# Performance work log

Measured on AMD Instinct MI355X. Metric: run time of the kernel, lower is better.

## Reference

```python
import jax, jax.numpy as jnp
import numpy as np

DEPTH, HEADS, DIM, DHEAD, MLP = 4, 16, 1024, 64, 4096
B, N, M = 4, 1024, 1024
EPS = 1e-5


def layer_norm(x, w, b):
    mu = jnp.mean(x, axis=-1, keepdims=True)
    var = jnp.var(x, axis=-1, keepdims=True)
    return (x - mu) * jax.lax.rsqrt(var + EPS) * w + b


def setup_inputs() -> dict:
    key = jax.random.key(0)
    ks = jax.random.split(key, 16)
    inner = HEADS * DHEAD
    s = lambda fan_in: 1.0 / np.sqrt(fan_in)
    # weights stored in (in, out) layout: y = x @ W + b
    return {
        "x": jax.random.normal(ks[0], (B, N, DIM), jnp.float32),
        "m": jax.random.normal(ks[1], (B, M, DIM), jnp.float32),
        "Wq": jax.random.normal(ks[2], (DEPTH, DIM, inner), jnp.float32) * s(DIM),
        "Wk": jax.random.normal(ks[3], (DEPTH, DIM, inner), jnp.float32) * s(DIM),
        "Wv": jax.random.normal(ks[4], (DEPTH, DIM, inner), jnp.float32) * s(DIM),
        "Wo": jax.random.normal(ks[5], (DEPTH, inner, DIM), jnp.float32) * s(inner),
        "bo": jnp.zeros((DEPTH, DIM), jnp.float32),
        "ln1_w": jnp.ones((DEPTH, DIM), jnp.float32),
        "ln1_b": jnp.zeros((DEPTH, DIM), jnp.float32),
        "W1": jax.random.normal(ks[6], (DEPTH, DIM, MLP), jnp.float32) * s(DIM),
        "b1": jnp.zeros((DEPTH, MLP), jnp.float32),
        "W2": jax.random.normal(ks[7], (DEPTH, MLP, DIM), jnp.float32) * s(MLP),
        "b2": jnp.zeros((DEPTH, DIM), jnp.float32),
        "ln2_w": jnp.ones((DEPTH, DIM), jnp.float32),
        "ln2_b": jnp.zeros((DEPTH, DIM), jnp.float32),
    }


def reference(x, m, Wq, Wk, Wv, Wo, bo, ln1_w, ln1_b, W1, b1, W2, b2, ln2_w, ln2_b):
    scale = DIM ** (-0.5)  # NOTE: original scales by dim**-0.5, not dim_head**-0.5
    for i in range(DEPTH):
        # cross-attention block (PreNorm on x only; m is used raw, as in source)
        h = layer_norm(x, ln1_w[i], ln1_b[i])
        q = jnp.einsum('bnd,de->bne', h, Wq[i]).reshape(B, N, HEADS, DHEAD)
        k = jnp.einsum('bmd,de->bme', m, Wk[i]).reshape(B, M, HEADS, DHEAD)
        v = jnp.einsum('bmd,de->bme', m, Wv[i]).reshape(B, M, HEADS, DHEAD)
        dots = jnp.einsum('bihd,bjhd->bhij', q, k) * scale
        attn = jax.nn.softmax(dots, axis=-1)
        out = jnp.einsum('bhij,bjhd->bihd', attn, v).reshape(B, N, HEADS * DHEAD)
        x = x + jnp.einsum('bne,ed->bnd', out, Wo[i]) + bo[i]
        # feed-forward block
        h2 = layer_norm(x, ln2_w[i], ln2_b[i])
        ff = jax.nn.gelu(jnp.einsum('bnd,df->bnf', h2, W1[i]) + b1[i], approximate=False)
        x = x + jnp.einsum('bnf,fd->bnd', ff, W2[i]) + b2[i]
    return x
```

## Files before the change

### kernel.cpp

```cpp
#include <hip/hip_runtime.h>
#include <hip/hip_bf16.h>
#include <math.h>

typedef __hip_bfloat16 bf16;
typedef __attribute__((ext_vector_type(8))) short bf16x8;
typedef __attribute__((ext_vector_type(4))) float f32x4;

#define DEPTH  4
#define HEADS  16
#define DIM    1024
#define DHEAD  64
#define MLPD   4096
#define BB     4
#define NN     1024
#define MMK    1024
#define ROWS   (BB*NN)
#define QKVS   3072

__device__ inline float bitsbf(short s) {
  union { float f; unsigned u; } c; c.u = ((unsigned)(unsigned short)s) << 16; return c.f;
}
__device__ inline short bfbits(float f) {
  bf16 h = __float2bfloat16(f); return *(short*)&h;
}

__device__ inline void gload_lds16(const bf16* g, bf16* l) {
  __builtin_amdgcn_global_load_lds((const __attribute__((address_space(1))) unsigned int*)g,
                                   (__attribute__((address_space(3))) unsigned int*)l, 16, 0, 0);
}

__global__ __launch_bounds__(256) void f2b_kernel(const float* __restrict__ in, bf16* __restrict__ out, int n) {
  int i = blockIdx.x * 256 + threadIdx.x;
  if (i < n) out[i] = __float2bfloat16(in[i]);
}

__global__ __launch_bounds__(256) void transpose_f2b(const float* __restrict__ in, bf16* __restrict__ out,
                                                     int inStride, int rowOff, int colOff, int outStride) {
  __shared__ float tile[32][33];
  int n0 = blockIdx.x * 32, k0 = blockIdx.y * 32;
  int tx = threadIdx.x, ty = threadIdx.y;
  #pragma unroll
  for (int i = 0; i < 32; i += 8)
    tile[ty + i][tx] = in[(size_t)(rowOff + k0 + ty + i) * inStride + colOff + n0 + tx];
  __syncthreads();
  #pragma unroll
  for (int i = 0; i < 32; i += 8)
    out[(size_t)(n0 + ty + i) * outStride + k0 + tx] = __float2bfloat16(tile[tx][ty + i]);
}

__global__ __launch_bounds__(256) void ln_kernel(const float* __restrict__ x, const float* __restrict__ w,
                                                 const float* __restrict__ b, bf16* __restrict__ out) {
  int row = blockIdx.x, t = threadIdx.x;
  const float* xr = x + (size_t)row * DIM;
  float4 xv = *(const float4*)(xr + t * 4);
  float s  = xv.x + xv.y + xv.z + xv.w;
  float s2 = xv.x * xv.x + xv.y * xv.y + xv.z * xv.z + xv.w * xv.w;
  #pragma unroll
  for (int off = 32; off; off >>= 1) { s += __shfl_xor(s, off, 64); s2 += __shfl_xor(s2, off, 64); }
  __shared__ float sh_s[4], sh_s2[4], sh_mu, sh_rstd;
  int wid = t >> 6;
  if ((t & 63) == 0) { sh_s[wid] = s; sh_s2[wid] = s2; }
  __syncthreads();
  if (t == 0) {
    float S1 = sh_s[0] + sh_s[1] + sh_s[2] + sh_s[3];
    float S2 = sh_s2[0] + sh_s2[1] + sh_s2[2] + sh_s2[3];
    float mu = S1 * (1.0f / DIM);
    float var = S2 * (1.0f / DIM) - mu * mu;
    sh_mu = mu; sh_rstd = rsqrtf(var + 1e-5f);
  }
  __syncthreads();
  float mu = sh_mu, rstd = sh_rstd;
  float4 wv = *(const float4*)(w + t * 4);
  float4 bv = *(const float4*)(b + t * 4);
  bf16* orow = out + (size_t)row * DIM + t * 4;
  orow[0] = __float2bfloat16((xv.x - mu) * rstd * wv.x + bv.x);
  orow[1] = __float2bfloat16((xv.y - mu) * rstd * wv.y + bv.y);
  orow[2] = __float2bfloat16((xv.z - mu) * rstd * wv.z + bv.z);
  orow[3] = __float2bfloat16((xv.w - mu) * rstd * wv.w + bv.w);
}

#define MODE_PLAIN 0
#define MODE_GELU  1
#define MODE_RES   2
#define BM 128
#define BK2 64

template<int JT>
__global__ __launch_bounds__(256) void gemm_tile(const bf16* __restrict__ A, const bf16* __restrict__ Bt,
                                                 const float* __restrict__ bias, bf16* __restrict__ outb,
                                                 float* __restrict__ resf, int outStride, int K, int mode) {
  constexpr int BN = JT * 32;
  __shared__ __align__(16) bf16 As[2][BM * BK2];
  __shared__ __align__(16) bf16 Bs[2][BN * BK2];
  int t = threadIdx.x;
  int w = t >> 6, l = t & 63;
  int l15 = l & 15, quad = l >> 4;
  int l8 = l & 7, lh = l >> 3;
  int col0 = blockIdx.x * BN, row0 = blockIdx.y * BM;
  int wm = (w >> 1) * 64, wn = (w & 1) * (JT * 16);

  f32x4 acc[4][JT] = {};

  int swk = (l8 ^ lh) * 8;
  const bf16* agB = A  + (size_t)(row0 + w * 32 + lh) * K + swk;
  const bf16* bgB = Bt + (size_t)(col0 + (JT == 4 ? w * 32 : w * 16) + lh) * K + swk;

  #pragma unroll
  for (int i = 0; i < 4; ++i)
    gload_lds16(agB + (size_t)(i * 8) * K, &As[0][w * 2048 + i * 512]);
  #pragma unroll
  for (int i = 0; i < (JT == 4 ? 4 : 2); ++i)
    gload_lds16(bgB + (size_t)(i * 8) * K, &Bs[0][w * (JT == 4 ? 2048 : 1024) + i * 512]);

  int cur = 0;
  for (int k0 = 0; k0 < K; k0 += BK2) {
    __syncthreads();
    int nxt = cur ^ 1;
    if (k0 + BK2 < K) {
      #pragma unroll
      for (int i = 0; i < 4; ++i)
        gload_lds16(agB + (size_t)(i * 8) * K + k0 + BK2, &As[nxt][w * 2048 + i * 512]);
      #pragma unroll
      for (int i = 0; i < (JT == 4 ? 4 : 2); ++i)
        gload_lds16(bgB + (size_t)(i * 8) * K + k0 + BK2, &Bs[nxt][w * (JT == 4 ? 2048 : 1024) + i * 512]);
    }
    #pragma unroll
    for (int ks2 = 0; ks2 < 2; ++ks2) {
      bf16x8 af[4], bfr[JT];
      #pragma unroll
      for (int i = 0; i < 4; ++i) {
        int R = wm + i * 16 + l15;
        af[i] = *(const bf16x8*)&As[cur][R * 64 + (((quad + 4 * ks2) ^ (l15 & 7)) * 8)];
      }
      #pragma unroll
      for (int j = 0; j < JT; ++j) {
        int R = wn + j * 16 + l15;
        bfr[j] = *(const bf16x8*)&Bs[cur][R * 64 + (((quad + 4 * ks2) ^ (l15 & 7)) * 8)];
      }
      #pragma unroll
      for (int i = 0; i < 4; ++i)
        #pragma unroll
        for (int j = 0; j < JT; ++j)
          acc[i][j] = __builtin_amdgcn_mfma_f32_16x16x32_bf16(af[i], bfr[j], acc[i][j], 0, 0, 0);
    }
    cur = nxt;
  }

  #pragma unroll
  for (int i = 0; i < 4; ++i) {
    #pragma unroll
    for (int j = 0; j < JT; ++j) {
      int gcol = col0 + wn + j * 16 + l15;
      float bval = (mode != MODE_PLAIN && bias != nullptr) ? bias[gcol] : 0.0f;
      #pragma unroll
      for (int r = 0; r < 4; ++r) {
        int grow = row0 + wm + i * 16 + quad * 4 + r;
        float val = acc[i][j][r];
        size_t idx = (size_t)grow * outStride + gcol;
        if (mode == MODE_RES) {
          resf[idx] = resf[idx] + val + bval;
        } else {
          if (mode == MODE_GELU) {
            float u = val + bval;
            val = 0.5f * u * (1.0f + erff(u * 0.70710678118654752f));
          }
          outb[idx] = __float2bfloat16(val);
        }
      }
    }
  }
}

#define ALDP 72

__global__ __launch_bounds__(256) void attn_mfma_kernel(const bf16* __restrict__ qkv, bf16* __restrict__ o) {
  __shared__ __align__(16) bf16  Kl[2][64 * 64];
  __shared__ __align__(16) short Vt[2][64][ALDP];
  __shared__ __align__(16) short Pl[64][ALDP];

  int t = threadIdx.x;
  int lane = t & 63, w = t >> 6;
  int l15 = lane & 15, quad = lane >> 4;
  int bh = blockIdx.x;
  int qt = blockIdx.y;
  int b = bh >> 4, hh = bh & 15;

  const bf16* q = qkv;
  const bf16* k = qkv + 1024;
  const bf16* v = qkv + 2048;

  int krow = w * 16 + (lane >> 3);
  int kcol = ((lane & 7) ^ (lane >> 3)) * 8;
  const bf16* kg0 = k + (size_t)(b * MMK + krow) * QKVS + hh * DHEAD + kcol;
  const bf16* kg1 = kg0 + (size_t)8 * QKVS;

  int srow = t >> 2, sc0 = (t & 3) * 16;
  const bf16* vg = v + (size_t)(b * MMK + srow) * QKVS + hh * DHEAD + sc0;

  bf16x8 qfrag[2];
  {
    const bf16* qp = q + (size_t)(b * NN + qt * 64 + w * 16 + l15) * QKVS + hh * DHEAD + quad * 8;
    #pragma unroll
    for (int ks = 0; ks < 2; ++ks) {
      bf16x8 raw = *(const bf16x8*)(qp + ks * 32);
      bf16x8 sc;
      #pragma unroll
      for (int e = 0; e < 8; ++e) sc[e] = bfbits(bitsbf(raw[e]) * 0.03125f);
      qfrag[ks] = sc;
    }
  }

  gload_lds16(kg0, &Kl[0][w * 1024]);
  gload_lds16(kg1, &Kl[0][w * 1024 + 512]);
  {
    bf16x8 v0 = *(const bf16x8*)vg;
    bf16x8 v1 = *(const bf16x8*)(vg + 8);
    #pragma unroll
    for (int e = 0; e < 8; ++e) {
      Vt[0][sc0 + e][srow]     = v0[e];
      Vt[0][sc0 + 8 + e][srow] = v1[e];
    }
  }

  f32x4 Oacc[4] = {{}, {}, {}, {}};
  float mrow[4] = {-1e30f, -1e30f, -1e30f, -1e30f};
  float lrow[4] = {0.f, 0.f, 0.f, 0.f};

  int cur = 0;
  for (int kt = 0; kt < MMK / 64; ++kt) {
    __syncthreads();
    int nxt = cur ^ 1;
    bool more = (kt + 1 < MMK / 64);
    bf16x8 nv0, nv1;
    if (more) {
      const bf16* vgn = vg + (size_t)(kt + 1) * 64 * QKVS;
      nv0 = *(const bf16x8*)vgn;
      nv1 = *(const bf16x8*)(vgn + 8);
      gload_lds16(kg0 + (size_t)(kt + 1) * 64 * QKVS, &Kl[nxt][w * 1024]);
      gload_lds16(kg1 + (size_t)(kt + 1) * 64 * QKVS, &Kl[nxt][w * 1024 + 512]);
    }

    f32x4 S[4] = {{}, {}, {}, {}};
    #pragma unroll
    for (int ks = 0; ks < 2; ++ks) {
      #pragma unroll
      for (int j = 0; j < 4; ++j) {
        bf16x8 bfr = *(const bf16x8*)&Kl[cur][(j * 16 + l15) * 64 + (((ks * 4 + quad) ^ (l15 & 7)) * 8)];
        S[j] = __builtin_amdgcn_mfma_f32_16x16x32_bf16(qfrag[ks], bfr, S[j], 0, 0, 0);
      }
    }

    #pragma unroll
    for (int r = 0; r < 4; ++r) {
      float tm = fmaxf(fmaxf(S[0][r], S[1][r]), fmaxf(S[2][r], S[3][r]));
      tm = fmaxf(tm, __shfl_xor(tm, 1, 64));
      tm = fmaxf(tm, __shfl_xor(tm, 2, 64));
      tm = fmaxf(tm, __shfl_xor(tm, 4, 64));
      tm = fmaxf(tm, __shfl_xor(tm, 8, 64));
      float mn = fmaxf(mrow[r], tm);
      float alpha = __expf(mrow[r] - mn);
      mrow[r] = mn;
      float rs = 0.f;
      #pragma unroll
      for (int j = 0; j < 4; ++j) {
        float p = __expf(S[j][r] - mn);
        S[j][r] = p;
        rs += p;
      }
      rs += __shfl_xor(rs, 1, 64);
      rs += __shfl_xor(rs, 2, 64);
      rs += __shfl_xor(rs, 4, 64);
      rs += __shfl_xor(rs, 8, 64);
      lrow[r] = lrow[r] * alpha + rs;
      #pragma unroll
      for (int j = 0; j < 4; ++j) {
        Oacc[j][r] *= alpha;
        Pl[w * 16 + quad * 4 + r][j * 16 + l15] = bfbits(S[j][r]);
      }
    }

    #pragma unroll
    for (int ks = 0; ks < 2; ++ks) {
      bf16x8 pa = *(const bf16x8*)&Pl[w * 16 + l15][ks * 32 + quad * 8];
      #pragma unroll
      for (int j = 0; j < 4; ++j) {
        bf16x8 vb = *(const bf16x8*)&Vt[cur][j * 16 + l15][ks * 32 + quad * 8];
        Oacc[j] = __builtin_amdgcn_mfma_f32_16x16x32_bf16(pa, vb, Oacc[j], 0, 0, 0);
      }
    }

    if (more) {
      #pragma unroll
      for (int e = 0; e < 8; ++e) {
        Vt[nxt][sc0 + e][srow]     = nv0[e];
        Vt[nxt][sc0 + 8 + e][srow] = nv1[e];
      }
    }
    cur = nxt;
  }

  #pragma unroll
  for (int r = 0; r < 4; ++r) {
    float inv = 1.0f / lrow[r];
    bf16* op = o + (size_t)(b * NN + qt * 64 + w * 16 + quad * 4 + r) * DIM + hh * DHEAD;
    #pragma unroll
    for (int j = 0; j < 4; ++j)
      op[j * 16 + l15] = __float2bfloat16(Oacc[j][r] * inv);
  }
}

extern "C" void kernel_launch(void* const* d_in, const int* in_sizes, int n_in,
                              void* d_out, int out_size, void* d_ws, size_t ws_size,
                              hipStream_t stream) {
  const float* x_in = (const float*)d_in[0];
  const float* m    = (const float*)d_in[1];
  const float* Wq   = (const float*)d_in[2];
  const float* Wk   = (const float*)d_in[3];
  const float* Wv   = (const float*)d_in[4];
  const float* Wo   = (const float*)d_in[5];
  const float* bo   = (const float*)d_in[6];
  const float* ln1w = (const float*)d_in[7];
  const float* ln1b = (const float*)d_in[8];
  const float* W1   = (const float*)d_in[9];
  const float* b1   = (const float*)d_in[10];
  const float* W2   = (const float*)d_in[11];
  const float* b2   = (const float*)d_in[12];
  const float* ln2w = (const float*)d_in[13];
  const float* ln2b = (const float*)d_in[14];

  float* xf = (float*)d_out;

  char* ws = (char*)d_ws;
  bf16* h    = (bf16*)(ws + 0);
  bf16* mb   = (bf16*)(ws + (8u  << 20));
  bf16* qkv  = (bf16*)(ws + (16u << 20));
  bf16* ffh  = (bf16*)(ws + (16u << 20));
  bf16* wt   = (bf16*)(ws + (40u << 20));

  const int NTOK = ROWS * DIM;

  hipMemcpyAsync(xf, x_in, (size_t)NTOK * sizeof(float), hipMemcpyDeviceToDevice, stream);
  f2b_kernel<<<dim3((NTOK + 255) / 256), dim3(256), 0, stream>>>(m, mb, NTOK);

  dim3 blk(256);
  dim3 tblk(32, 8);
  dim3 g_n1(DIM / 64, ROWS / BM);
  dim3 g_n2(2048 / 128, ROWS / BM);
  dim3 tr_1k(DIM / 32, DIM / 32);
  dim3 tr_w1(2048 / 32, DIM / 32);
  dim3 tr_w2(DIM / 32, 2048 / 32);
  dim3 attn_grid(BB * HEADS, NN / 64);

  for (int L = 0; L < DEPTH; ++L) {
    const float* WqL = Wq + (size_t)L * DIM * DIM;
    const float* WkL = Wk + (size_t)L * DIM * DIM;
    const float* WvL = Wv + (size_t)L * DIM * DIM;
    const float* WoL = Wo + (size_t)L * DIM * DIM;
    const float* W1L = W1 + (size_t)L * DIM * MLPD;
    const float* W2L = W2 + (size_t)L * MLPD * DIM;

    ln_kernel<<<dim3(ROWS), blk, 0, stream>>>(xf, ln1w + L * DIM, ln1b + L * DIM, h);

    transpose_f2b<<<tr_1k, tblk, 0, stream>>>(WkL, wt, DIM, 0, 0, DIM);
    transpose_f2b<<<tr_1k, tblk, 0, stream>>>(WvL, wt + 1024 * 1024, DIM, 0, 0, DIM);
    gemm_tile<4><<<g_n2, blk, 0, stream>>>(mb, wt, nullptr, qkv + 1024, nullptr, QKVS, DIM, MODE_PLAIN);

    transpose_f2b<<<tr_1k, tblk, 0, stream>>>(WqL, wt, DIM, 0, 0, DIM);
    gemm_tile<2><<<g_n1, blk, 0, stream>>>(h, wt, nullptr, qkv, nullptr, QKVS, DIM, MODE_PLAIN);

    attn_mfma_kernel<<<attn_grid, blk, 0, stream>>>(qkv, h);

    transpose_f2b<<<tr_1k, tblk, 0, stream>>>(WoL, wt, DIM, 0, 0, DIM);
    gemm_tile<2><<<g_n1, blk, 0, stream>>>(h, wt, bo + L * DIM, nullptr, xf, DIM, DIM, MODE_RES);

    ln_kernel<<<dim3(ROWS), blk, 0, stream>>>(xf, ln2w + L * DIM, ln2b + L * DIM, h);

    for (int half = 0; half < 2; ++half) {
      transpose_f2b<<<tr_w1, tblk, 0, stream>>>(W1L, wt, MLPD, 0, half * 2048, DIM);
      gemm_tile<4><<<g_n2, blk, 0, stream>>>(h, wt, b1 + (size_t)L * MLPD + half * 2048, ffh, nullptr,
                                             2048, DIM, MODE_GELU);
      transpose_f2b<<<tr_w2, tblk, 0, stream>>>(W2L, wt, DIM, half * 2048, 0, 2048);
      gemm_tile<2><<<g_n1, blk, 0, stream>>>(ffh, wt, (half == 0) ? (b2 + (size_t)L * DIM) : nullptr,
                                             nullptr, xf, DIM, 2048, MODE_RES);
    }
  }
}
```

Measured before the change: 1.549 ms.

## Write V transposed from KV GEMM epilogue and read K/V directly in attention

The KV projection GEMM now writes V into a per-head transposed layout (head, dim, key) and K into a compact Q/K buffer with stride 2048. The attention kernel drops its LDS staging, double buffering and in-kernel V transpose, and loads K and V fragments straight from global memory. This removes LDS transpose work and barriers. In exchange, the transposed V stores in the GEMM epilogue are scattered, and the attention loop loses its prefetch overlap, so global load latency is exposed to each block.

```diff
diff --git a/kernel.cpp b/kernel.cpp
--- a/kernel.cpp
+++ b/kernel.cpp
@@ -15,7 +15,7 @@
 #define NN     1024
 #define MMK    1024
 #define ROWS   (BB*NN)
-#define QKVS   3072
+#define QKS    2048
 
 __device__ inline float bitsbf(short s) {
   union { float f; unsigned u; } c; c.u = ((unsigned)(unsigned short)s) << 16; return c.f;
@@ -82,13 +82,15 @@
 #define MODE_PLAIN 0
 #define MODE_GELU  1
 #define MODE_RES   2
+#define MODE_KVT   3
 #define BM 128
 #define BK2 64
 
 template<int JT>
 __global__ __launch_bounds__(256) void gemm_tile(const bf16* __restrict__ A, const bf16* __restrict__ Bt,
                                                  const float* __restrict__ bias, bf16* __restrict__ outb,
-                                                 float* __restrict__ resf, int outStride, int K, int mode) {
+                                                 float* __restrict__ resf, bf16* __restrict__ vtb,
+                                                 int outStride, int K, int mode) {
   constexpr int BN = JT * 32;
   __shared__ __align__(16) bf16 As[2][BM * BK2];
   __shared__ __align__(16) bf16 Bs[2][BN * BK2];
@@ -151,20 +153,30 @@
     #pragma unroll
     for (int j = 0; j < JT; ++j) {
       int gcol = col0 + wn + j * 16 + l15;
-      float bval = (mode != MODE_PLAIN && bias != nullptr) ? bias[gcol] : 0.0f;
+      float bval = ((mode == MODE_GELU || mode == MODE_RES) && bias != nullptr) ? bias[gcol] : 0.0f;
       #pragma unroll
       for (int r = 0; r < 4; ++r) {
         int grow = row0 + wm + i * 16 + quad * 4 + r;
         float val = acc[i][j][r];
-        size_t idx = (size_t)grow * outStride + gcol;
-        if (mode == MODE_RES) {
-          resf[idx] = resf[idx] + val + bval;
+        if (mode == MODE_KVT) {
+          if (gcol < 1024) {
+            outb[(size_t)grow * QKS + 1024 + gcol] = __float2bfloat16(val);
+          } else {
+            int vd = gcol - 1024, vh = vd >> 6, dl = vd & 63;
+            int bb2 = grow >> 10, key = grow & 1023;
+            vtb[((size_t)((bb2 * 16 + vh) * 64 + dl)) * 1024 + key] = __float2bfloat16(val);
+          }
         } else {
-          if (mode == MODE_GELU) {
-            float u = val + bval;
-            val = 0.5f * u * (1.0f + erff(u * 0.70710678118654752f));
+          size_t idx = (size_t)grow * outStride + gcol;
+          if (mode == MODE_RES) {
+            resf[idx] = resf[idx] + val + bval;
+          } else {
+            if (mode == MODE_GELU) {
+              float u = val + bval;
+              val = 0.5f * u * (1.0f + erff(u * 0.70710678118654752f));
+            }
+            outb[idx] = __float2bfloat16(val);
           }
-          outb[idx] = __float2bfloat16(val);
         }
       }
     }
@@ -173,9 +185,9 @@
 
 #define ALDP 72
 
-__global__ __launch_bounds__(256) void attn_mfma_kernel(const bf16* __restrict__ qkv, bf16* __restrict__ o) {
-  __shared__ __align__(16) bf16  Kl[2][64 * 64];
-  __shared__ __align__(16) short Vt[2][64][ALDP];
+__global__ __launch_bounds__(256) void attn_mfma_kernel(const bf16* __restrict__ qk,
+                                                        const bf16* __restrict__ vT,
+                                                        bf16* __restrict__ o) {
   __shared__ __align__(16) short Pl[64][ALDP];
 
   int t = threadIdx.x;
@@ -185,21 +197,9 @@
   int qt = blockIdx.y;
   int b = bh >> 4, hh = bh & 15;
 
-  const bf16* q = qkv;
-  const bf16* k = qkv + 1024;
-  const bf16* v = qkv + 2048;
-
-  int krow = w * 16 + (lane >> 3);
-  int kcol = ((lane & 7) ^ (lane >> 3)) * 8;
-  const bf16* kg0 = k + (size_t)(b * MMK + krow) * QKVS + hh * DHEAD + kcol;
-  const bf16* kg1 = kg0 + (size_t)8 * QKVS;
-
-  int srow = t >> 2, sc0 = (t & 3) * 16;
-  const bf16* vg = v + (size_t)(b * MMK + srow) * QKVS + hh * DHEAD + sc0;
-
   bf16x8 qfrag[2];
   {
-    const bf16* qp = q + (size_t)(b * NN + qt * 64 + w * 16 + l15) * QKVS + hh * DHEAD + quad * 8;
+    const bf16* qp = qk + (size_t)(b * NN + qt * 64 + w * 16 + l15) * QKS + hh * DHEAD + quad * 8;
     #pragma unroll
     for (int ks = 0; ks < 2; ++ks) {
       bf16x8 raw = *(const bf16x8*)(qp + ks * 32);
@@ -210,45 +210,26 @@
     }
   }
 
-  gload_lds16(kg0, &Kl[0][w * 1024]);
-  gload_lds16(kg1, &Kl[0][w * 1024 + 512]);
-  {
-    bf16x8 v0 = *(const bf16x8*)vg;
-    bf16x8 v1 = *(const bf16x8*)(vg + 8);
-    #pragma unroll
-    for (int e = 0; e < 8; ++e) {
-      Vt[0][sc0 + e][srow]     = v0[e];
-      Vt[0][sc0 + 8 + e][srow] = v1[e];
-    }
-  }
+  const bf16* kb = qk + (size_t)(b * MMK) * QKS + 1024 + hh * DHEAD + quad * 8;
+  const bf16* vb0 = vT + ((size_t)(b * 1024 + hh * 64)) * 1024;
 
   f32x4 Oacc[4] = {{}, {}, {}, {}};
   float mrow[4] = {-1e30f, -1e30f, -1e30f, -1e30f};
   float lrow[4] = {0.f, 0.f, 0.f, 0.f};
 
-  int cur = 0;
   for (int kt = 0; kt < MMK / 64; ++kt) {
-    __syncthreads();
-    int nxt = cur ^ 1;
-    bool more = (kt + 1 < MMK / 64);
-    bf16x8 nv0, nv1;
-    if (more) {
-      const bf16* vgn = vg + (size_t)(kt + 1) * 64 * QKVS;
-      nv0 = *(const bf16x8*)vgn;
-      nv1 = *(const bf16x8*)(vgn + 8);
-      gload_lds16(kg0 + (size_t)(kt + 1) * 64 * QKVS, &Kl[nxt][w * 1024]);
-      gload_lds16(kg1 + (size_t)(kt + 1) * 64 * QKVS, &Kl[nxt][w * 1024 + 512]);
-    }
-
     f32x4 S[4] = {{}, {}, {}, {}};
-    #pragma unroll
-    for (int ks = 0; ks < 2; ++ks) {
-      #pragma unroll
-      for (int j = 0; j < 4; ++j) {
-        bf16x8 bfr = *(const bf16x8*)&Kl[cur][(j * 16 + l15) * 64 + (((ks * 4 + quad) ^ (l15 & 7)) * 8)];
-        S[j] = __builtin_amdgcn_mfma_f32_16x16x32_bf16(qfrag[ks], bfr, S[j], 0, 0, 0);
-      }
-    }
+    bf16x8 kf[2][4];
+    #pragma unroll
+    for (int ks = 0; ks < 2; ++ks)
+      #pragma unroll
+      for (int j = 0; j < 4; ++j)
+        kf[ks][j] = *(const bf16x8*)(kb + (size_t)(kt * 64 + j * 16 + l15) * QKS + ks * 32);
+    #pragma unroll
+    for (int ks = 0; ks < 2; ++ks)
+      #pragma unroll
+      for (int j = 0; j < 4; ++j)
+        S[j] = __builtin_amdgcn_mfma_f32_16x16x32_bf16(qfrag[ks], kf[ks][j], S[j], 0, 0, 0);
 
     #pragma unroll
     for (int r = 0; r < 4; ++r) {
@@ -284,19 +265,10 @@
       bf16x8 pa = *(const bf16x8*)&Pl[w * 16 + l15][ks * 32 + quad * 8];
       #pragma unroll
       for (int j = 0; j < 4; ++j) {
-        bf16x8 vb = *(const bf16x8*)&Vt[cur][j * 16 + l15][ks * 32 + quad * 8];
-        Oacc[j] = __builtin_amdgcn_mfma_f32_16x16x32_bf16(pa, vb, Oacc[j], 0, 0, 0);
-      }
-    }
-
-    if (more) {
-      #pragma unroll
-      for (int e = 0; e < 8; ++e) {
-        Vt[nxt][sc0 + e][srow]     = nv0[e];
-        Vt[nxt][sc0 + 8 + e][srow] = nv1[e];
-      }
-    }
-    cur = nxt;
+        bf16x8 vf = *(const bf16x8*)(vb0 + (size_t)(j * 16 + l15) * 1024 + kt * 64 + ks * 32 + quad * 8);
+        Oacc[j] = __builtin_amdgcn_mfma_f32_16x16x32_bf16(pa, vf, Oacc[j], 0, 0, 0);
+      }
+    }
   }
 
   #pragma unroll
@@ -333,8 +305,9 @@
   char* ws = (char*)d_ws;
   bf16* h    = (bf16*)(ws + 0);
   bf16* mb   = (bf16*)(ws + (8u  << 20));
-  bf16* qkv  = (bf16*)(ws + (16u << 20));
+  bf16* qk   = (bf16*)(ws + (16u << 20));
   bf16* ffh  = (bf16*)(ws + (16u << 20));
+  bf16* vT   = (bf16*)(ws + (32u << 20));
   bf16* wt   = (bf16*)(ws + (40u << 20));
 
   const int NTOK = ROWS * DIM;
@@ -363,25 +336,25 @@
 
     transpose_f2b<<<tr_1k, tblk, 0, stream>>>(WkL, wt, DIM, 0, 0, DIM);
     transpose_f2b<<<tr_1k, tblk, 0, stream>>>(WvL, wt + 1024 * 1024, DIM, 0, 0, DIM);
-    gemm_tile<4><<<g_n2, blk, 0, stream>>>(mb, wt, nullptr, qkv + 1024, nullptr, QKVS, DIM, MODE_PLAIN);
+    gemm_tile<4><<<g_n2, blk, 0, stream>>>(mb, wt, nullptr, qk, nullptr, vT, QKS, DIM, MODE_KVT);
 
     transpose_f2b<<<tr_1k, tblk, 0, stream>>>(WqL, wt, DIM, 0, 0, DIM);
-    gemm_tile<2><<<g_n1, blk, 0, stream>>>(h, wt, nullptr, qkv, nullptr, QKVS, DIM, MODE_PLAIN);
-
-    attn_mfma_kernel<<<attn_grid, blk, 0, stream>>>(qkv, h);
+    gemm_tile<2><<<g_n1, blk, 0, stream>>>(h, wt, nullptr, qk, nullptr, nullptr, QKS, DIM, MODE_PLAIN);
+
+    attn_mfma_kernel<<<attn_grid, blk, 0, stream>>>(qk, vT, h);
 
     transpose_f2b<<<tr_1k, tblk, 0, stream>>>(WoL, wt, DIM, 0, 0, DIM);
-    gemm_tile<2><<<g_n1, blk, 0, stream>>>(h, wt, bo + L * DIM, nullptr, xf, DIM, DIM, MODE_RES);
+    gemm_tile<2><<<g_n1, blk, 0, stream>>>(h, wt, bo + L * DIM, nullptr, xf, nullptr, DIM, DIM, MODE_RES);
 
     ln_kernel<<<dim3(ROWS), blk, 0, stream>>>(xf, ln2w + L * DIM, ln2b + L * DIM, h);
 
     for (int half = 0; half < 2; ++half) {
       transpose_f2b<<<tr_w1, tblk, 0, stream>>>(W1L, wt, MLPD, 0, half * 2048, DIM);
       gemm_tile<4><<<g_n2, blk, 0, stream>>>(h, wt, b1 + (size_t)L * MLPD + half * 2048, ffh, nullptr,
-                                             2048, DIM, MODE_GELU);
+                                             nullptr, 2048, DIM, MODE_GELU);
       transpose_f2b<<<tr_w2, tblk, 0, stream>>>(W2L, wt, DIM, half * 2048, 0, 2048);
       gemm_tile<2><<<g_n1, blk, 0, stream>>>(ffh, wt, (half == 0) ? (b2 + (size_t)L * DIM) : nullptr,
-                                             nullptr, xf, DIM, 2048, MODE_RES);
-    }
-  }
-}
+                                             nullptr, xf, nullptr, DIM, 2048, MODE_RES);
+    }
+  }
+}
```

Measured after the change: 1.806 ms. 1.17x slower.
